# Kernel tuning notes

Measured on AMD Instinct MI355X. Metric: run time of the kernel, lower is better.

## Reference

```python
import jax, jax.numpy as jnp
import numpy as np

_BIG = 1e9  # effectively-infinite distance seed (float32-safe: _BIG**2 < f32 max)


def _dist1d(feature):
    """Exact 1D distance along axis 1 (H) to nearest True pixel. feature: [B,H,W] bool."""
    B, H, W = feature.shape
    seed = jnp.where(feature, 0.0, _BIG).astype(jnp.float32)  # [B,H,W]
    seq = jnp.moveaxis(seed, 1, 0)  # [H,B,W]

    def step(carry, s):
        c = jnp.minimum(carry + 1.0, s)
        return c, c

    init = jnp.full((B, W), _BIG, jnp.float32)
    _, fwd = jax.lax.scan(step, init, seq)
    _, bwd = jax.lax.scan(step, init, seq[::-1])
    d = jnp.minimum(fwd, bwd[::-1])  # [H,B,W]
    return jnp.moveaxis(d, 0, 1)  # [B,H,W]


def _edt(feature):
    """Exact 2D Euclidean distance to nearest True pixel (classic separable EDT:
    dt(i,j)^2 = min_j' ( d1(i,j')^2 + (j-j')^2 ), d1 = exact 1D distance along H).
    Matches scipy.ndimage.distance_transform_edt on ~feature's zero set."""
    d1 = _dist1d(feature)  # [B,H,W]
    W = d1.shape[-1]
    j = jnp.arange(W, dtype=jnp.float32)
    D2 = (j[:, None] - j[None, :]) ** 2  # [W(out), W(src)]
    g2 = d1 * d1  # [B,H,W]

    def row(g2_row):  # g2_row: [B,W] -> [B,W]; keeps peak intermediate at [B,W,W]
        return jnp.min(g2_row[:, None, :] + D2[None, :, :], axis=-1)

    dt2 = jax.lax.map(row, jnp.moveaxis(g2, 1, 0))  # [H,B,W]
    return jnp.sqrt(jnp.moveaxis(dt2, 0, 1))  # [B,H,W]


def setup_inputs() -> dict:
    key = jax.random.key(0)
    k1, k2 = jax.random.split(key)
    logits = jax.random.normal(k1, (16, 1, 512, 512), dtype=jnp.float32)
    targets = jax.random.uniform(k2, (16, 1, 512, 512), dtype=jnp.float32)
    return {"logits": logits, "targets": targets}


def reference(logits, targets):
    probs = jnp.clip(jax.nn.sigmoid(logits), 1e-7, 1.0 - 1e-7)
    t = targets[:, 0] > 0.5  # [B,H,W] bool
    # scipy: edt(t==0) = dist-to-(t==1) set; edt(t==1) = dist-to-(t==0) set
    dt = _edt(t) + _edt(~t)  # [B,H,W]
    dt = jax.lax.stop_gradient(dt)[:, None]  # [B,1,H,W], detached like torch
    return jnp.mean(probs * dt)
```

## Files before the change

kernel.cpp:

```cpp
#include <hip/hip_runtime.h>
#include <cstdint>

#define BB 16
#define HH 512
#define WW 512
#define NPIX (BB*HH*WW)
#define WR (HH/32)
#define NWORDS (BB*WR*WW)
#define NXCD 8
#define RPB 8
#define NPAIR (RPB/2)
#define NGRP (BB*HH/RPB)
#define GCHUNK (NGRP/NXCD)

__global__ __launch_bounds__(256) void packbits(const float* __restrict__ targets,
                                                uint32_t* __restrict__ vmask) {
    const int flat = blockIdx.x * 256 + threadIdx.x;
    const int jp = (flat & 255) * 2;
    const int w  = (flat >> 8) & (WR - 1);
    const int b  = flat >> 12;
    const float2* base =
        (const float2*)(targets + ((size_t)(b * HH + w * 32)) * WW + jp);
    uint32_t w0 = 0, w1 = 0;
    #pragma unroll
    for (int r = 0; r < 32; ++r) {
        const float2 q = base[r * (WW / 2)];
        w0 |= (q.x > 0.5f ? 1u : 0u) << r;
        w1 |= (q.y > 0.5f ? 1u : 0u) << r;
    }
    ((uint2*)vmask)[flat] = make_uint2(w0, w1);
}

__global__ __launch_bounds__(512) void fused_row8(
        const uint32_t* __restrict__ vmask,
        const float* __restrict__ logits,
        float* __restrict__ partial) {
    const int bid = blockIdx.x;
    const int g   = (bid & (NXCD - 1)) * GCHUNK + (bid >> 3);
    const int b   = g >> 6;
    const int i0  = (g & 63) << 3;
    const int j   = threadIdx.x;
    const int w   = i0 >> 5;
    const int p0  = i0 & 31;

    __shared__ uint32_t pk_s[NPAIR][WW];
    __shared__ float    sw[8];

    const uint32_t* vm = vmask + (size_t)b * WR * WW;

    const uint32_t Wse = vm[w * WW + j];
    const bool has_u = (w > 0), has_d = (w < WR - 1);
    const uint32_t Wup = has_u ? vm[(w - 1) * WW + j] : 0u;
    const uint32_t Wdn = has_d ? vm[(w + 1) * WW + j] : 0u;

    float xs[RPB];
    #pragma unroll
    for (int r = 0; r < RPB; ++r)
        xs[r] = logits[((size_t)(b * HH + i0 + r)) * WW + j];

    const uint64_t downfull = (uint64_t)Wse | ((uint64_t)Wdn << 32);
    const uint64_t upfull   = ((uint64_t)Wse << 32) | (uint64_t)Wup;
    const uint64_t Td = (downfull ^ (downfull >> 1)) &
                        (has_d ? 0x7FFFFFFFFFFFFFFFull : 0x000000007FFFFFFFull);
    const uint64_t Tu = (upfull ^ (upfull >> 1)) &
                        (has_u ? 0xFFFFFFFFFFFFFFFFull : 0xFFFFFFFF00000000ull);

    int dpx[RPB], tpx[RPB];
    #pragma unroll
    for (int r = 0; r < RPB; ++r) {
        const int p = p0 + r;
        const int i = i0 + r;
        const int t = (int)((Wse >> p) & 1u);

        const uint64_t zd = Td >> p;
        const uint64_t zu = Tu << (32 - p);
        int dd, du;
        if (zd) {
            dd = __ffsll((unsigned long long)zd);
        } else {
            const uint32_t tm = t ? 0xFFFFFFFFu : 0u;
            dd = 1023;
            for (int ww = w + 2; ww < WR; ++ww) {
                const uint32_t Xw = vm[ww * WW + j] ^ tm;
                if (Xw) { dd = 32 * ww + (__ffs(Xw) - 1) - i; break; }
            }
        }
        if (zu) {
            du = __clzll((long long)zu) + 1;
        } else {
            const uint32_t tm = t ? 0xFFFFFFFFu : 0u;
            du = 1023;
            for (int ww = w - 2; ww >= 0; --ww) {
                const uint32_t Xw = vm[ww * WW + j] ^ tm;
                if (Xw) { du = i - (32 * ww + 31 - __clz((int)Xw)); break; }
            }
        }
        dpx[r] = min(min(dd, du), 1023);
        tpx[r] = t;
    }

    #pragma unroll
    for (int pr = 0; pr < NPAIR; ++pr) {
        const uint32_t lo = (uint32_t)((dpx[2 * pr]     << 1) | tpx[2 * pr]);
        const uint32_t hi = (uint32_t)((dpx[2 * pr + 1] << 1) | tpx[2 * pr + 1]);
        pk_s[pr][j] = lo | (hi << 16);
    }
    __syncthreads();

    int mpx[RPB];
    #pragma unroll
    for (int pr = 0; pr < NPAIR; ++pr) {
        const int t0 = tpx[2 * pr], t1 = tpx[2 * pr + 1];
        int m0 = dpx[2 * pr] * dpx[2 * pr];
        int m1 = dpx[2 * pr + 1] * dpx[2 * pr + 1];
        const uint32_t* rowp = &pk_s[pr][0];

        #pragma unroll
        for (int k = 1; k <= 2; ++k) {
            const int jl = j - k, jr = j + k;
            const int k2 = k * k;
            const uint32_t pl = rowp[jl >= 0 ? jl : 0];
            const uint32_t pr_ = rowp[jr < WW ? jr : (WW - 1)];
            const int d0l = ((int)(pl & 1u) == t0)          ? (int)((pl & 0xFFFFu) >> 1) : 0;
            const int d1l = ((int)((pl >> 16) & 1u) == t1)  ? (int)(pl >> 17)            : 0;
            const int d0r = ((int)(pr_ & 1u) == t0)         ? (int)((pr_ & 0xFFFFu) >> 1) : 0;
            const int d1r = ((int)((pr_ >> 16) & 1u) == t1) ? (int)(pr_ >> 17)           : 0;
            const int c0l = (jl >= 0) ? (d0l * d0l + k2) : 0x7fffffff;
            const int c1l = (jl >= 0) ? (d1l * d1l + k2) : 0x7fffffff;
            const int c0r = (jr < WW) ? (d0r * d0r + k2) : 0x7fffffff;
            const int c1r = (jr < WW) ? (d1r * d1r + k2) : 0x7fffffff;
            m0 = min(m0, min(c0l, c0r));
            m1 = min(m1, min(c1l, c1r));
        }

        {
            const int kmaxRow = max(j, WW - 1 - j);
            for (int k = 3; k <= kmaxRow && k * k < max(m0, m1); ++k) {
                const int k2 = k * k;
                if (k <= j) {
                    const uint32_t p2 = rowp[j - k];
                    const int e0 = ((int)(p2 & 1u) == t0)         ? (int)((p2 & 0xFFFFu) >> 1) : 0;
                    const int e1 = ((int)((p2 >> 16) & 1u) == t1) ? (int)(p2 >> 17)            : 0;
                    m0 = min(m0, e0 * e0 + k2);
                    m1 = min(m1, e1 * e1 + k2);
                }
                if (k <= WW - 1 - j) {
                    const uint32_t p2 = rowp[j + k];
                    const int e0 = ((int)(p2 & 1u) == t0)         ? (int)((p2 & 0xFFFFu) >> 1) : 0;
                    const int e1 = ((int)((p2 >> 16) & 1u) == t1) ? (int)(p2 >> 17)            : 0;
                    m0 = min(m0, e0 * e0 + k2);
                    m1 = min(m1, e1 * e1 + k2);
                }
            }
        }
        mpx[2 * pr] = m0;
        mpx[2 * pr + 1] = m1;
    }

    float v = 0.0f;
    #pragma unroll
    for (int r = 0; r < RPB; ++r) {
        const float dt = __builtin_amdgcn_sqrtf((float)mpx[r]);
        float pr = __builtin_amdgcn_rcpf(1.0f + __expf(-xs[r]));
        pr = fminf(fmaxf(pr, 1e-7f), (float)(1.0 - 1e-7));
        v += pr * dt;
    }

    #pragma unroll
    for (int off = 32; off > 0; off >>= 1)
        v += __shfl_down(v, off);

    const int lane = threadIdx.x & 63;
    const int wid  = threadIdx.x >> 6;
    if (lane == 0) sw[wid] = v;
    __syncthreads();
    if (threadIdx.x == 0) {
        float s = 0.0f;
        #pragma unroll
        for (int ww = 0; ww < 8; ++ww) s += sw[ww];
        partial[g] = s;
    }
}

__global__ __launch_bounds__(256) void finalreduce(
        const float* __restrict__ partial,
        float* __restrict__ out) {
    const float4 q = ((const float4*)partial)[threadIdx.x];
    float v = (q.x + q.y) + (q.z + q.w);

    #pragma unroll
    for (int off = 32; off > 0; off >>= 1)
        v += __shfl_down(v, off);

    __shared__ float sw[4];
    const int lane = threadIdx.x & 63;
    const int wid  = threadIdx.x >> 6;
    if (lane == 0) sw[wid] = v;
    __syncthreads();
    if (threadIdx.x == 0)
        out[0] = ((sw[0] + sw[1]) + (sw[2] + sw[3])) * (1.0f / (float)NPIX);
}

extern "C" void kernel_launch(void* const* d_in, const int* in_sizes, int n_in,
                              void* d_out, int out_size, void* d_ws, size_t ws_size,
                              hipStream_t stream) {
    const float* logits  = (const float*)d_in[0];
    const float* targets = (const float*)d_in[1];
    float* out = (float*)d_out;

    uint32_t* vmask = (uint32_t*)d_ws;
    float* partial  = (float*)((char*)d_ws + (size_t)NWORDS * sizeof(uint32_t));

    packbits<<<NWORDS / 2 / 256, 256, 0, stream>>>(targets, vmask);
    fused_row8<<<NGRP, 512, 0, stream>>>(vmask, logits, partial);
    finalreduce<<<1, 256, 0, stream>>>(partial, out);
}
```

Baseline: 20.77 us.

## Fuse bit-packing into main kernel processing 32-row bands per block

Removes the separate packbits kernel: each block now builds column bitmasks directly from the float targets for its 32-row band and the neighbouring bands, then processes the band in four 8-row chunks. This removes one kernel launch and the vmask round trip through global memory. In exchange, targets are re-read by neighbouring blocks and the grid shrinks to 256 blocks, each doing serial work with extra barriers. The final reduction is cut to a single wavefront.

```diff
diff --git a/kernel.cpp b/kernel.cpp
--- a/kernel.cpp
+++ b/kernel.cpp
@@ -5,58 +5,41 @@
 #define HH 512
 #define WW 512
 #define NPIX (BB*HH*WW)
-#define WR (HH/32)
-#define NWORDS (BB*WR*WW)
+#define NBLK 256
 #define NXCD 8
-#define RPB 8
-#define NPAIR (RPB/2)
-#define NGRP (BB*HH/RPB)
-#define GCHUNK (NGRP/NXCD)
-
-__global__ __launch_bounds__(256) void packbits(const float* __restrict__ targets,
-                                                uint32_t* __restrict__ vmask) {
-    const int flat = blockIdx.x * 256 + threadIdx.x;
-    const int jp = (flat & 255) * 2;
-    const int w  = (flat >> 8) & (WR - 1);
-    const int b  = flat >> 12;
-    const float2* base =
-        (const float2*)(targets + ((size_t)(b * HH + w * 32)) * WW + jp);
-    uint32_t w0 = 0, w1 = 0;
-    #pragma unroll
-    for (int r = 0; r < 32; ++r) {
-        const float2 q = base[r * (WW / 2)];
-        w0 |= (q.x > 0.5f ? 1u : 0u) << r;
-        w1 |= (q.y > 0.5f ? 1u : 0u) << r;
-    }
-    ((uint2*)vmask)[flat] = make_uint2(w0, w1);
-}
-
-__global__ __launch_bounds__(512) void fused_row8(
-        const uint32_t* __restrict__ vmask,
+
+__global__ __launch_bounds__(512) void fused32(
+        const float* __restrict__ targets,
         const float* __restrict__ logits,
         float* __restrict__ partial) {
     const int bid = blockIdx.x;
-    const int g   = (bid & (NXCD - 1)) * GCHUNK + (bid >> 3);
-    const int b   = g >> 6;
-    const int i0  = (g & 63) << 3;
+    const int g   = (bid & (NXCD - 1)) * (NBLK / NXCD) + (bid >> 3);
+    const int b   = g >> 4;
+    const int w   = g & 15;
+    const int i0  = w << 5;
     const int j   = threadIdx.x;
-    const int w   = i0 >> 5;
-    const int p0  = i0 & 31;
-
-    __shared__ uint32_t pk_s[NPAIR][WW];
+
+    __shared__ uint32_t pk_s[4][WW];
     __shared__ float    sw[8];
 
-    const uint32_t* vm = vmask + (size_t)b * WR * WW;
-
-    const uint32_t Wse = vm[w * WW + j];
-    const bool has_u = (w > 0), has_d = (w < WR - 1);
-    const uint32_t Wup = has_u ? vm[(w - 1) * WW + j] : 0u;
-    const uint32_t Wdn = has_d ? vm[(w + 1) * WW + j] : 0u;
-
-    float xs[RPB];
+    const float* tcol = targets + (size_t)b * HH * WW + j;
+    const float* lcol = logits  + (size_t)b * HH * WW + j;
+    const bool has_u = (w > 0), has_d = (w < 15);
+
+    uint32_t Wse = 0u, Wup = 0u, Wdn = 0u;
     #pragma unroll
-    for (int r = 0; r < RPB; ++r)
-        xs[r] = logits[((size_t)(b * HH + i0 + r)) * WW + j];
+    for (int r = 0; r < 32; ++r)
+        Wse |= (tcol[(i0 + r) * WW] > 0.5f ? 1u : 0u) << r;
+    if (has_u) {
+        #pragma unroll
+        for (int r = 0; r < 32; ++r)
+            Wup |= (tcol[(i0 - 32 + r) * WW] > 0.5f ? 1u : 0u) << r;
+    }
+    if (has_d) {
+        #pragma unroll
+        for (int r = 0; r < 32; ++r)
+            Wdn |= (tcol[(i0 + 32 + r) * WW] > 0.5f ? 1u : 0u) << r;
+    }
 
     const uint64_t downfull = (uint64_t)Wse | ((uint64_t)Wdn << 32);
     const uint64_t upfull   = ((uint64_t)Wse << 32) | (uint64_t)Wup;
@@ -65,105 +48,113 @@
     const uint64_t Tu = (upfull ^ (upfull >> 1)) &
                         (has_u ? 0xFFFFFFFFFFFFFFFFull : 0xFFFFFFFF00000000ull);
 
-    int dpx[RPB], tpx[RPB];
-    #pragma unroll
-    for (int r = 0; r < RPB; ++r) {
-        const int p = p0 + r;
-        const int i = i0 + r;
-        const int t = (int)((Wse >> p) & 1u);
-
-        const uint64_t zd = Td >> p;
-        const uint64_t zu = Tu << (32 - p);
-        int dd, du;
-        if (zd) {
-            dd = __ffsll((unsigned long long)zd);
-        } else {
-            const uint32_t tm = t ? 0xFFFFFFFFu : 0u;
-            dd = 1023;
-            for (int ww = w + 2; ww < WR; ++ww) {
-                const uint32_t Xw = vm[ww * WW + j] ^ tm;
-                if (Xw) { dd = 32 * ww + (__ffs(Xw) - 1) - i; break; }
-            }
-        }
-        if (zu) {
-            du = __clzll((long long)zu) + 1;
-        } else {
-            const uint32_t tm = t ? 0xFFFFFFFFu : 0u;
-            du = 1023;
-            for (int ww = w - 2; ww >= 0; --ww) {
-                const uint32_t Xw = vm[ww * WW + j] ^ tm;
-                if (Xw) { du = i - (32 * ww + 31 - __clz((int)Xw)); break; }
-            }
-        }
-        dpx[r] = min(min(dd, du), 1023);
-        tpx[r] = t;
-    }
-
-    #pragma unroll
-    for (int pr = 0; pr < NPAIR; ++pr) {
-        const uint32_t lo = (uint32_t)((dpx[2 * pr]     << 1) | tpx[2 * pr]);
-        const uint32_t hi = (uint32_t)((dpx[2 * pr + 1] << 1) | tpx[2 * pr + 1]);
-        pk_s[pr][j] = lo | (hi << 16);
-    }
-    __syncthreads();
-
-    int mpx[RPB];
-    #pragma unroll
-    for (int pr = 0; pr < NPAIR; ++pr) {
-        const int t0 = tpx[2 * pr], t1 = tpx[2 * pr + 1];
-        int m0 = dpx[2 * pr] * dpx[2 * pr];
-        int m1 = dpx[2 * pr + 1] * dpx[2 * pr + 1];
-        const uint32_t* rowp = &pk_s[pr][0];
-
-        #pragma unroll
-        for (int k = 1; k <= 2; ++k) {
-            const int jl = j - k, jr = j + k;
-            const int k2 = k * k;
-            const uint32_t pl = rowp[jl >= 0 ? jl : 0];
-            const uint32_t pr_ = rowp[jr < WW ? jr : (WW - 1)];
-            const int d0l = ((int)(pl & 1u) == t0)          ? (int)((pl & 0xFFFFu) >> 1) : 0;
-            const int d1l = ((int)((pl >> 16) & 1u) == t1)  ? (int)(pl >> 17)            : 0;
-            const int d0r = ((int)(pr_ & 1u) == t0)         ? (int)((pr_ & 0xFFFFu) >> 1) : 0;
-            const int d1r = ((int)((pr_ >> 16) & 1u) == t1) ? (int)(pr_ >> 17)           : 0;
-            const int c0l = (jl >= 0) ? (d0l * d0l + k2) : 0x7fffffff;
-            const int c1l = (jl >= 0) ? (d1l * d1l + k2) : 0x7fffffff;
-            const int c0r = (jr < WW) ? (d0r * d0r + k2) : 0x7fffffff;
-            const int c1r = (jr < WW) ? (d1r * d1r + k2) : 0x7fffffff;
-            m0 = min(m0, min(c0l, c0r));
-            m1 = min(m1, min(c1l, c1r));
-        }
-
-        {
-            const int kmaxRow = max(j, WW - 1 - j);
-            for (int k = 3; k <= kmaxRow && k * k < max(m0, m1); ++k) {
+    float v = 0.0f;
+
+    for (int c = 0; c < 4; ++c) {
+        const int p0 = c << 3;
+
+        float xs[8];
+        #pragma unroll
+        for (int r = 0; r < 8; ++r)
+            xs[r] = lcol[(i0 + p0 + r) * WW];
+
+        int dpx[8], tpx[8];
+        #pragma unroll
+        for (int r = 0; r < 8; ++r) {
+            const int p = p0 + r;
+            const int i = i0 + p;
+            const int t = (int)((Wse >> p) & 1u);
+            const uint64_t zd = Td >> p;
+            const uint64_t zu = Tu << (32 - p);
+            int dd, du;
+            if (zd) {
+                dd = __ffsll((unsigned long long)zd);
+            } else {
+                dd = 1023;
+                for (int i2 = 32 * w + 64; i2 < HH; ++i2) {
+                    const int t2 = tcol[i2 * WW] > 0.5f ? 1 : 0;
+                    if (t2 != t) { dd = i2 - i; break; }
+                }
+            }
+            if (zu) {
+                du = __clzll((long long)zu) + 1;
+            } else {
+                du = 1023;
+                for (int i2 = 32 * w - 33; i2 >= 0; --i2) {
+                    const int t2 = tcol[i2 * WW] > 0.5f ? 1 : 0;
+                    if (t2 != t) { du = i - i2; break; }
+                }
+            }
+            dpx[r] = min(min(dd, du), 1023);
+            tpx[r] = t;
+        }
+
+        #pragma unroll
+        for (int pr = 0; pr < 4; ++pr) {
+            const uint32_t lo = (uint32_t)((dpx[2 * pr]     << 1) | tpx[2 * pr]);
+            const uint32_t hi = (uint32_t)((dpx[2 * pr + 1] << 1) | tpx[2 * pr + 1]);
+            pk_s[pr][j] = lo | (hi << 16);
+        }
+        __syncthreads();
+
+        int mpx[8];
+        #pragma unroll
+        for (int pr = 0; pr < 4; ++pr) {
+            const int t0 = tpx[2 * pr], t1 = tpx[2 * pr + 1];
+            int m0 = dpx[2 * pr] * dpx[2 * pr];
+            int m1 = dpx[2 * pr + 1] * dpx[2 * pr + 1];
+            const uint32_t* rowp = &pk_s[pr][0];
+
+            #pragma unroll
+            for (int k = 1; k <= 2; ++k) {
+                const int jl = j - k, jr = j + k;
                 const int k2 = k * k;
-                if (k <= j) {
-                    const uint32_t p2 = rowp[j - k];
-                    const int e0 = ((int)(p2 & 1u) == t0)         ? (int)((p2 & 0xFFFFu) >> 1) : 0;
-                    const int e1 = ((int)((p2 >> 16) & 1u) == t1) ? (int)(p2 >> 17)            : 0;
-                    m0 = min(m0, e0 * e0 + k2);
-                    m1 = min(m1, e1 * e1 + k2);
+                const uint32_t pl  = rowp[jl >= 0 ? jl : 0];
+                const uint32_t pr_ = rowp[jr < WW ? jr : (WW - 1)];
+                const int d0l = ((int)(pl & 1u) == t0)          ? (int)((pl & 0xFFFFu) >> 1)  : 0;
+                const int d1l = ((int)((pl >> 16) & 1u) == t1)  ? (int)(pl >> 17)             : 0;
+                const int d0r = ((int)(pr_ & 1u) == t0)         ? (int)((pr_ & 0xFFFFu) >> 1) : 0;
+                const int d1r = ((int)((pr_ >> 16) & 1u) == t1) ? (int)(pr_ >> 17)            : 0;
+                const int c0l = (jl >= 0) ? (d0l * d0l + k2) : 0x7fffffff;
+                const int c1l = (jl >= 0) ? (d1l * d1l + k2) : 0x7fffffff;
+                const int c0r = (jr < WW) ? (d0r * d0r + k2) : 0x7fffffff;
+                const int c1r = (jr < WW) ? (d1r * d1r + k2) : 0x7fffffff;
+                m0 = min(m0, min(c0l, c0r));
+                m1 = min(m1, min(c1l, c1r));
+            }
+
+            {
+                const int kmaxRow = max(j, WW - 1 - j);
+                for (int k = 3; k <= kmaxRow && k * k < max(m0, m1); ++k) {
+                    const int k2 = k * k;
+                    if (k <= j) {
+                        const uint32_t p2 = rowp[j - k];
+                        const int e0 = ((int)(p2 & 1u) == t0)         ? (int)((p2 & 0xFFFFu) >> 1) : 0;
+                        const int e1 = ((int)((p2 >> 16) & 1u) == t1) ? (int)(p2 >> 17)            : 0;
+                        m0 = min(m0, e0 * e0 + k2);
+                        m1 = min(m1, e1 * e1 + k2);
+                    }
+                    if (k <= WW - 1 - j) {
+                        const uint32_t p2 = rowp[j + k];
+                        const int e0 = ((int)(p2 & 1u) == t0)         ? (int)((p2 & 0xFFFFu) >> 1) : 0;
+                        const int e1 = ((int)((p2 >> 16) & 1u) == t1) ? (int)(p2 >> 17)            : 0;
+                        m0 = min(m0, e0 * e0 + k2);
+                        m1 = min(m1, e1 * e1 + k2);
+                    }
                 }
-                if (k <= WW - 1 - j) {
-                    const uint32_t p2 = rowp[j + k];
-                    const int e0 = ((int)(p2 & 1u) == t0)         ? (int)((p2 & 0xFFFFu) >> 1) : 0;
-                    const int e1 = ((int)((p2 >> 16) & 1u) == t1) ? (int)(p2 >> 17)            : 0;
-                    m0 = min(m0, e0 * e0 + k2);
-                    m1 = min(m1, e1 * e1 + k2);
-                }
-            }
-        }
-        mpx[2 * pr] = m0;
-        mpx[2 * pr + 1] = m1;
-    }
-
-    float v = 0.0f;
-    #pragma unroll
-    for (int r = 0; r < RPB; ++r) {
-        const float dt = __builtin_amdgcn_sqrtf((float)mpx[r]);
-        float pr = __builtin_amdgcn_rcpf(1.0f + __expf(-xs[r]));
-        pr = fminf(fmaxf(pr, 1e-7f), (float)(1.0 - 1e-7));
-        v += pr * dt;
+            }
+            mpx[2 * pr]     = m0;
+            mpx[2 * pr + 1] = m1;
+        }
+        __syncthreads();
+
+        #pragma unroll
+        for (int r = 0; r < 8; ++r) {
+            const float dt = __builtin_amdgcn_sqrtf((float)mpx[r]);
+            float pr = __builtin_amdgcn_rcpf(1.0f + __expf(-xs[r]));
+            pr = fminf(fmaxf(pr, 1e-7f), (float)(1.0 - 1e-7));
+            v += pr * dt;
+        }
     }
 
     #pragma unroll
@@ -182,7 +173,7 @@
     }
 }
 
-__global__ __launch_bounds__(256) void finalreduce(
+__global__ __launch_bounds__(64) void finalreduce(
         const float* __restrict__ partial,
         float* __restrict__ out) {
     const float4 q = ((const float4*)partial)[threadIdx.x];
@@ -192,13 +183,8 @@
     for (int off = 32; off > 0; off >>= 1)
         v += __shfl_down(v, off);
 
-    __shared__ float sw[4];
-    const int lane = threadIdx.x & 63;
-    const int wid  = threadIdx.x >> 6;
-    if (lane == 0) sw[wid] = v;
-    __syncthreads();
     if (threadIdx.x == 0)
-        out[0] = ((sw[0] + sw[1]) + (sw[2] + sw[3])) * (1.0f / (float)NPIX);
+        out[0] = v * (1.0f / (float)NPIX);
 }
 
 extern "C" void kernel_launch(void* const* d_in, const int* in_sizes, int n_in,
@@ -208,10 +194,8 @@
     const float* targets = (const float*)d_in[1];
     float* out = (float*)d_out;
 
-    uint32_t* vmask = (uint32_t*)d_ws;
-    float* partial  = (float*)((char*)d_ws + (size_t)NWORDS * sizeof(uint32_t));
-
-    packbits<<<NWORDS / 2 / 256, 256, 0, stream>>>(targets, vmask);
-    fused_row8<<<NGRP, 512, 0, stream>>>(vmask, logits, partial);
-    finalreduce<<<1, 256, 0, stream>>>(partial, out);
+    float* partial = (float*)d_ws;
+
+    fused32<<<NBLK, 512, 0, stream>>>(targets, logits, partial);
+    finalreduce<<<1, 64, 0, stream>>>(partial, out);
 }
```

Result: no change. 20.68 us (-0.4%).
